# Kernel optimization log

Hardware: AMD Instinct MI355X
Metric: run time of the kernel (lower is better)

## Reference

```python
import jax, jax.numpy as jnp
import numpy as np

B, S, D, H, FF = 2, 2048, 1024, 16, 4096
DH = D // H  # head dim


def _layernorm(x, g, b, eps=1e-5):
    m = x.mean(-1, keepdims=True)
    v = ((x - m) ** 2).mean(-1, keepdims=True)
    return (x - m) / jnp.sqrt(v + eps) * g + b


def setup_inputs() -> dict:
    key = jax.random.key(0)
    ks = jax.random.split(key, 10)
    s = 0.02
    return {
        "x": jax.random.normal(ks[0], (B, S, D), jnp.float32),
        "y": jax.random.normal(ks[1], (B, S, D), jnp.float32),
        "z": jax.random.normal(ks[2], (B, S, D), jnp.float32),
        "mask": jnp.ones((B, 1, S, S), jnp.int32),
        "Wq": jax.random.normal(ks[3], (D, D), jnp.float32) * s,
        "bq": jnp.zeros((D,), jnp.float32),
        "Wk": jax.random.normal(ks[4], (D, D), jnp.float32) * s,
        "bk": jnp.zeros((D,), jnp.float32),
        "Wv": jax.random.normal(ks[5], (D, D), jnp.float32) * s,
        "bv": jnp.zeros((D,), jnp.float32),
        "Wo": jax.random.normal(ks[6], (D, D), jnp.float32) * s,
        "bo": jnp.zeros((D,), jnp.float32),
        "W1": jax.random.normal(ks[7], (D, FF), jnp.float32) * s,
        "b1": jnp.zeros((FF,), jnp.float32),
        "W2": jax.random.normal(ks[8], (FF, D), jnp.float32) * s,
        "b2": jnp.zeros((D,), jnp.float32),
        "ln_g": jnp.ones((D,), jnp.float32),
        "ln_b": jnp.zeros((D,), jnp.float32),
    }


def reference(x, y, z, mask, Wq, bq, Wk, bk, Wv, bv, Wo, bo, W1, b1, W2, b2, ln_g, ln_b):
    q = (x @ Wq + bq).reshape(B, S, H, DH)
    k = (y @ Wk + bk).reshape(B, S, H, DH)
    v = (z @ Wv + bv).reshape(B, S, H, DH)
    # scores: [B, H, Q, K]
    scores = jnp.einsum('bqhl,bkhl->bhqk', q, k) / (DH ** 0.5)
    scores = jnp.where(mask == 0, jnp.float32(-1e10), scores)
    # NOTE: source softmaxes over dim=2 (the query axis) -- faithful.
    p = jax.nn.softmax(scores, axis=2)
    # Source einsum 'bhqk,bvhl->bvhl' sums p over q,k -> per-(b,h) scalar scaling v.
    s_bh = p.sum(axis=(2, 3))  # [B, H]
    att = s_bh[:, None, :, None] * v  # [B, S, H, DH]
    att = att.reshape(B, S, D) @ Wo + bo
    # shared AddAndNorm (same LayerNorm params used twice); dropout = identity (eval)
    h1 = _layernorm(z + att, ln_g, ln_b)
    ff = jax.nn.relu(h1 @ W1 + b1) @ W2 + b2
    return _layernorm(h1 + ff, ln_g, ln_b)
```

## Files before the change

kernel.cpp:

```cpp
#include <hip/hip_runtime.h>

static constexpr int kB = 2, kS = 2048, kD = 1024, kFF = 4096;
static constexpr int kM = kB * kS;
static constexpr size_t MB = 1u << 20;

typedef __attribute__((ext_vector_type(8))) short short8;
typedef __attribute__((ext_vector_type(8))) unsigned short ushort8;
typedef __attribute__((ext_vector_type(4))) float f32x4;

__device__ __forceinline__ unsigned short f2bf(float f) {
  union { float f; unsigned int u; } c; c.f = f;
  unsigned int u = c.u;
  unsigned int r = u + 0x7FFFu + ((u >> 16) & 1u);
  return (unsigned short)(r >> 16);
}

__device__ __forceinline__ float bf2f(unsigned short b) {
  union { unsigned int u; float f; } c;
  c.u = ((unsigned int)b) << 16;
  return c.f;
}

__device__ __forceinline__ void gload_lds16(const void* g, void* l) {
  __builtin_amdgcn_global_load_lds(
      (const __attribute__((address_space(1))) void*)g,
      (__attribute__((address_space(3))) void*)l, 16, 0, 0);
}

__device__ __forceinline__ void do_ct64(
    const float* __restrict__ W, unsigned short* __restrict__ Wt,
    int K, int N, float scale, int ntN, int b, float (*tile)[65]) {
  const int nb = (b % ntN) * 64, kb = (b / ntN) * 64;
  const int tx = threadIdx.x & 15, ty = threadIdx.x >> 4;
#pragma unroll
  for (int p = 0; p < 4; ++p) {
    const int r = ty + 16 * p;
    float4 v = *(const float4*)(W + (size_t)(kb + r) * N + nb + tx * 4);
    tile[r][tx * 4 + 0] = v.x;
    tile[r][tx * 4 + 1] = v.y;
    tile[r][tx * 4 + 2] = v.z;
    tile[r][tx * 4 + 3] = v.w;
  }
  __syncthreads();
#pragma unroll
  for (int p = 0; p < 4; ++p) {
    const int n = ty + 16 * p;
    ushort4 o;
    o.x = f2bf(tile[tx * 4 + 0][n] * scale);
    o.y = f2bf(tile[tx * 4 + 1][n] * scale);
    o.z = f2bf(tile[tx * 4 + 2][n] * scale);
    o.w = f2bf(tile[tx * 4 + 3][n] * scale);
    *(ushort4*)(Wt + (size_t)(nb + n) * K + kb + tx * 4) = o;
  }
}

__global__ __launch_bounds__(256) void prep_kernel(
    const float* __restrict__ Wo, const float* __restrict__ Wv,
    const float* __restrict__ W1, const float* __restrict__ W2,
    const float* __restrict__ bv,
    unsigned short* __restrict__ WoT, unsigned short* __restrict__ WvBf,
    unsigned short* __restrict__ W1T, unsigned short* __restrict__ W2T,
    float* __restrict__ bprt) {
  __shared__ float tile[64][65];
  const int b = blockIdx.x;
  if (b < 256) {
    do_ct64(Wo, WoT, kD, kD, (float)kS, 16, b, tile);
  } else if (b < 1280) {
    do_ct64(W1, W1T, kD, kFF, 1.0f, 64, b - 256, tile);
  } else if (b < 2304) {
    do_ct64(W2, W2T, kFF, kD, 1.0f, 16, b - 1280, tile);
  } else if (b < 3328) {
    const int i = ((b - 2304) * 256 + threadIdx.x) * 4;
    float4 v = *(const float4*)(Wv + i);
    ushort4 o;
    o.x = f2bf(v.x); o.y = f2bf(v.y); o.z = f2bf(v.z); o.w = f2bf(v.w);
    *(ushort4*)(WvBf + i) = o;
  } else {
    const int bb = b - 3328, t = threadIdx.x;
    const int c = t * 4;
    float4 acc = {0.f, 0.f, 0.f, 0.f};
#pragma unroll
    for (int r = 0; r < 8; ++r) {
      const int f = bb * 8 + r;
      const float s = bv[f];
      float4 w = *(const float4*)(Wo + (size_t)f * 1024 + c);
      acc.x = fmaf(s, w.x, acc.x);
      acc.y = fmaf(s, w.y, acc.y);
      acc.z = fmaf(s, w.z, acc.z);
      acc.w = fmaf(s, w.w, acc.w);
    }
    *(float4*)(bprt + (size_t)bb * 1024 + c) = acc;
  }
}

__global__ __launch_bounds__(256) void combine_wc4_fin_kernel(
    const unsigned short* __restrict__ P, unsigned short* __restrict__ Wt,
    const float* __restrict__ bprt, const float* __restrict__ bo,
    float* __restrict__ bc) {
  const int i = (blockIdx.x * 256 + threadIdx.x) * 4;
  const int MN = 1024 * 1024;
  ushort4 s0 = *(const ushort4*)(P + i);
  ushort4 s1 = *(const ushort4*)(P + MN + i);
  ushort4 s2 = *(const ushort4*)(P + 2 * MN + i);
  ushort4 s3 = *(const ushort4*)(P + 3 * MN + i);
  const int row = i >> 10, col = i & 1023;
  float v0 = bf2f(s0.x) + bf2f(s1.x) + bf2f(s2.x) + bf2f(s3.x) + (row == col + 0 ? 1.0f : 0.0f);
  float v1 = bf2f(s0.y) + bf2f(s1.y) + bf2f(s2.y) + bf2f(s3.y) + (row == col + 1 ? 1.0f : 0.0f);
  float v2 = bf2f(s0.z) + bf2f(s1.z) + bf2f(s2.z) + bf2f(s3.z) + (row == col + 2 ? 1.0f : 0.0f);
  float v3 = bf2f(s0.w) + bf2f(s1.w) + bf2f(s2.w) + bf2f(s3.w) + (row == col + 3 ? 1.0f : 0.0f);
  ushort4 o; o.x = f2bf(v0); o.y = f2bf(v1); o.z = f2bf(v2); o.w = f2bf(v3);
  *(ushort4*)(Wt + i) = o;
  if (blockIdx.x < 4) {
    const int n = blockIdx.x * 256 + threadIdx.x;
    float acc = 0.0f;
#pragma unroll 8
    for (int bb = 0; bb < 128; ++bb) acc += bprt[(size_t)bb * 1024 + n];
    bc[n] = 2048.0f * acc + bo[n];
  }
}

template <int OUT_BF16, int RELU, int A_F32>
__global__ __launch_bounds__(256, 4) void gemm_bt(
    const void* __restrict__ A, const unsigned short* __restrict__ Bt,
    const float* __restrict__ bias, void* __restrict__ Cout,
    int M, int N, int K, int nXtiles, int nTilesPerSplit, int kSplitLen,
    size_t cStride, int cr, int cc) {
  __shared__ __align__(16) unsigned short sA[128 * 64];
  __shared__ __align__(16) unsigned short sB[128 * 64];
  const unsigned short* Ab = (const unsigned short*)A;
  const float* Af = (const float*)A;
  const int tid = threadIdx.x;
  const int wave = tid >> 6, lane = tid & 63;
  const int wr = wave >> 1, wc = wave & 1;

  const int x = blockIdx.x & 7, j = blockIdx.x >> 3;
  const int bpc = cr * cc;
  const int chunkIdx = x + 8 * (j / bpc);
  const int w = j % bpc;
  const int chunksPerSplit = nTilesPerSplit / bpc;
  const int split = chunkIdx / chunksPerSplit;
  const int cL = chunkIdx % chunksPerSplit;
  const int cpr = nXtiles / cc;
  const int m0 = ((cL / cpr) * cr + w / cc) * 128;
  const int n0 = ((cL % cpr) * cc + w % cc) * 128;
  const int kBeg = split * kSplitLen, kEnd = kBeg + kSplitLen;

  const int srow = lane >> 3;
  const int scol = ((lane & 7) ^ srow) * 8;

  f32x4 acc[4][4] = {};

  for (int k0 = kBeg; k0 < kEnd; k0 += 64) {
    if constexpr (A_F32) {
      float4 pa[4][2];
#pragma unroll
      for (int i = 0; i < 4; ++i) {
        const int chunk = i * 4 + wave;
        const int rr = chunk * 8 + srow;
        const float* az = Af + (size_t)(m0 + rr) * K + (k0 + scol);
        pa[i][0] = *(const float4*)az;
        pa[i][1] = *(const float4*)(az + 4);
      }
#pragma unroll
      for (int i = 0; i < 4; ++i) {
        const int chunk = i * 4 + wave;
        short8 cv;
        cv[0] = (short)f2bf(pa[i][0].x); cv[1] = (short)f2bf(pa[i][0].y);
        cv[2] = (short)f2bf(pa[i][0].z); cv[3] = (short)f2bf(pa[i][0].w);
        cv[4] = (short)f2bf(pa[i][1].x); cv[5] = (short)f2bf(pa[i][1].y);
        cv[6] = (short)f2bf(pa[i][1].z); cv[7] = (short)f2bf(pa[i][1].w);
        *(short8*)&sA[chunk * 512 + lane * 8] = cv;
      }
    } else {
#pragma unroll
      for (int i = 0; i < 4; ++i) {
        const int chunk = i * 4 + wave;
        const int rr = chunk * 8 + srow;
        gload_lds16(Ab + (size_t)(m0 + rr) * K + (k0 + scol), &sA[chunk * 512]);
      }
    }
#pragma unroll
    for (int i = 0; i < 4; ++i) {
      const int chunk = i * 4 + wave;
      const int rr = chunk * 8 + srow;
      gload_lds16(Bt + (size_t)(n0 + rr) * K + (k0 + scol), &sB[chunk * 512]);
    }
    __syncthreads();
#pragma unroll
    for (int kk = 0; kk < 64; kk += 32) {
      const int kcol = kk + (lane >> 4) * 8;
      const int kswz = (lane & 7) * 8;
      short8 af[4], bfr[4];
#pragma unroll
      for (int m = 0; m < 4; ++m)
        af[m] = *(const short8*)&sA[(wr * 64 + m * 16 + (lane & 15)) * 64 + (kcol ^ kswz)];
#pragma unroll
      for (int n = 0; n < 4; ++n)
        bfr[n] = *(const short8*)&sB[(wc * 64 + n * 16 + (lane & 15)) * 64 + (kcol ^ kswz)];
#pragma unroll
      for (int m = 0; m < 4; ++m)
#pragma unroll
        for (int n = 0; n < 4; ++n)
          acc[m][n] = __builtin_amdgcn_mfma_f32_16x16x32_bf16(af[m], bfr[n], acc[m][n], 0, 0, 0);
    }
    __syncthreads();
  }

  const int cl = lane & 15, rg = lane >> 4;
  const float* bptr = (split == 0) ? bias : nullptr;
#pragma unroll
  for (int n = 0; n < 4; ++n) {
    const int col = n0 + wc * 64 + n * 16 + cl;
    const float bias_v = bptr ? bptr[col] : 0.0f;
#pragma unroll
    for (int m = 0; m < 4; ++m) {
      const int rbase = m0 + wr * 64 + m * 16 + rg * 4;
#pragma unroll
      for (int j2 = 0; j2 < 4; ++j2) {
        float v = acc[m][n][j2] + bias_v;
        if (RELU) v = fmaxf(v, 0.0f);
        const size_t idx = split * cStride + (size_t)(rbase + j2) * N + col;
        if (OUT_BF16)
          ((unsigned short*)Cout)[idx] = f2bf(v);
        else
          ((float*)Cout)[idx] = v;
      }
    }
  }
}

__global__ __launch_bounds__(256) void ln4_wave_kernel(
    const unsigned short* __restrict__ P, size_t pStr,
    const float* __restrict__ gg, const float* __restrict__ bb,
    unsigned short* __restrict__ Hb) {
  const int wave = threadIdx.x >> 6, lane = threadIdx.x & 63;
  const int row = blockIdx.x * 4 + wave;
  const size_t rbase = (size_t)row * 1024;
  float a[16];
#pragma unroll
  for (int sw = 0; sw < 2; ++sw) {
    const size_t idx = rbase + sw * 512 + lane * 8;
    ushort8 v0 = *(const ushort8*)(P + idx);
    ushort8 v1 = *(const ushort8*)(P + pStr + idx);
    ushort8 v2 = *(const ushort8*)(P + 2 * pStr + idx);
    ushort8 v3 = *(const ushort8*)(P + 3 * pStr + idx);
#pragma unroll
    for (int j = 0; j < 8; ++j)
      a[sw * 8 + j] = bf2f(v0[j]) + bf2f(v1[j]) + bf2f(v2[j]) + bf2f(v3[j]);
  }
  float s = 0.f, ss = 0.f;
#pragma unroll
  for (int j = 0; j < 16; ++j) { s += a[j]; ss += a[j] * a[j]; }
#pragma unroll
  for (int off = 32; off > 0; off >>= 1) {
    s += __shfl_down(s, off);
    ss += __shfl_down(ss, off);
  }
  s = __shfl(s, 0);
  ss = __shfl(ss, 0);
  const float mean = s * (1.0f / 1024.0f);
  const float rstd = rsqrtf(ss * (1.0f / 1024.0f) - mean * mean + 1e-5f);
#pragma unroll
  for (int sw = 0; sw < 2; ++sw) {
    const int cbase = sw * 512 + lane * 8;
    float4 g0 = *(const float4*)(gg + cbase);
    float4 g1 = *(const float4*)(gg + cbase + 4);
    float4 b0 = *(const float4*)(bb + cbase);
    float4 b1 = *(const float4*)(bb + cbase + 4);
    const float* gp0 = &g0.x; const float* gp1 = &g1.x;
    const float* bp0 = &b0.x; const float* bp1 = &b1.x;
    ushort8 o;
#pragma unroll
    for (int j = 0; j < 4; ++j) {
      o[j]     = f2bf((a[sw * 8 + j]     - mean) * rstd * gp0[j] + bp0[j]);
      o[4 + j] = f2bf((a[sw * 8 + 4 + j] - mean) * rstd * gp1[j] + bp1[j]);
    }
    *(ushort8*)(Hb + rbase + cbase) = o;
  }
}

__global__ __launch_bounds__(256) void ln_fin_wave_kernel(
    const unsigned short* __restrict__ Res, const unsigned short* __restrict__ P,
    size_t pStr, const float* __restrict__ gg, const float* __restrict__ bb,
    float* __restrict__ out) {
  const int wave = threadIdx.x >> 6, lane = threadIdx.x & 63;
  const int row = blockIdx.x * 4 + wave;
  const size_t rbase = (size_t)row * 1024;
  float a[16];
#pragma unroll
  for (int sw = 0; sw < 2; ++sw) {
    const size_t idx = rbase + sw * 512 + lane * 8;
    ushort8 rv = *(const ushort8*)(Res + idx);
    ushort8 v0 = *(const ushort8*)(P + idx);
    ushort8 v1 = *(const ushort8*)(P + pStr + idx);
    ushort8 v2 = *(const ushort8*)(P + 2 * pStr + idx);
    ushort8 v3 = *(const ushort8*)(P + 3 * pStr + idx);
#pragma unroll
    for (int j = 0; j < 8; ++j)
      a[sw * 8 + j] = bf2f(rv[j]) + bf2f(v0[j]) + bf2f(v1[j]) + bf2f(v2[j]) + bf2f(v3[j]);
  }
  float s = 0.f, ss = 0.f;
#pragma unroll
  for (int j = 0; j < 16; ++j) { s += a[j]; ss += a[j] * a[j]; }
#pragma unroll
  for (int off = 32; off > 0; off >>= 1) {
    s += __shfl_down(s, off);
    ss += __shfl_down(ss, off);
  }
  s = __shfl(s, 0);
  ss = __shfl(ss, 0);
  const float mean = s * (1.0f / 1024.0f);
  const float rstd = rsqrtf(ss * (1.0f / 1024.0f) - mean * mean + 1e-5f);
#pragma unroll
  for (int sw = 0; sw < 2; ++sw) {
    const int cbase = sw * 512 + lane * 8;
    float4 g0 = *(const float4*)(gg + cbase);
    float4 g1 = *(const float4*)(gg + cbase + 4);
    float4 b0 = *(const float4*)(bb + cbase);
    float4 b1 = *(const float4*)(bb + cbase + 4);
    const float* gp0 = &g0.x; const float* gp1 = &g1.x;
    const float* bp0 = &b0.x; const float* bp1 = &b1.x;
    float4 o0, o1;
    float* op0 = &o0.x; float* op1 = &o1.x;
#pragma unroll
    for (int j = 0; j < 4; ++j) {
      op0[j] = (a[sw * 8 + j]     - mean) * rstd * gp0[j] + bp0[j];
      op1[j] = (a[sw * 8 + 4 + j] - mean) * rstd * gp1[j] + bp1[j];
    }
    *(float4*)(out + rbase + cbase) = o0;
    *(float4*)(out + rbase + cbase + 4) = o1;
  }
}

extern "C" void kernel_launch(void* const* d_in, const int* in_sizes, int n_in,
                              void* d_out, int out_size, void* d_ws, size_t ws_size,
                              hipStream_t stream) {
  const float* z  = (const float*)d_in[2];
  const float* Wv = (const float*)d_in[8];
  const float* bv = (const float*)d_in[9];
  const float* Wo = (const float*)d_in[10];
  const float* bo = (const float*)d_in[11];
  const float* W1 = (const float*)d_in[12];
  const float* b1 = (const float*)d_in[13];
  const float* W2 = (const float*)d_in[14];
  const float* b2 = (const float*)d_in[15];
  const float* lng = (const float*)d_in[16];
  const float* lnb = (const float*)d_in[17];
  float* out = (float*)d_out;

  char* ws = (char*)d_ws;
  unsigned short* a1   = (unsigned short*)(ws + 0 * MB);
  unsigned short* attP = (unsigned short*)(ws + 32 * MB);
  unsigned short* ffP  = (unsigned short*)(ws + 32 * MB);
  unsigned short* W2T  = (unsigned short*)(ws + 64 * MB);
  unsigned short* wcpB = (unsigned short*)(ws + 72 * MB);
  unsigned short* WoT  = (unsigned short*)(ws + 88 * MB);
  unsigned short* WvBf = (unsigned short*)(ws + 90 * MB);
  unsigned short* WcT  = (unsigned short*)(ws + 92 * MB);
  float*          bc   = (float*)(ws + 94 * MB);
  float*          bprt = (float*)(ws + 94 * MB + 65536);
  unsigned short* h1bf = (unsigned short*)(ws + 96 * MB);
  unsigned short* W1T  = (unsigned short*)(ws + 104 * MB);

  const size_t pStr = (size_t)kM * kD;
  const size_t wStr = (size_t)kD * kD;

  prep_kernel<<<dim3(3456), dim3(256), 0, stream>>>(
      Wo, Wv, W1, W2, bv, WoT, WvBf, W1T, W2T, bprt);

  gemm_bt<1, 0, 0><<<dim3(256), dim3(256), 0, stream>>>(
      WoT, WvBf, nullptr, wcpB, kD, kD, kD, kD / 128, 64, 256, wStr, 8, 4);

  combine_wc4_fin_kernel<<<dim3(1024), dim3(256), 0, stream>>>(
      wcpB, WcT, bprt, bo, bc);

  gemm_bt<1, 0, 1><<<dim3(1024), dim3(256), 0, stream>>>(
      z, WcT, bc, attP, kM, kD, kD, kD / 128, 256, 256, pStr, 8, 8);

  ln4_wave_kernel<<<dim3(kM / 4), dim3(256), 0, stream>>>(
      attP, pStr, lng, lnb, h1bf);

  gemm_bt<1, 1, 0><<<dim3(1024), dim3(256), 0, stream>>>(
      h1bf, W1T, b1, a1, kM, kFF, kD, kFF / 128, 1024, kD, 0, 16, 8);

  gemm_bt<1, 0, 0><<<dim3(1024), dim3(256), 0, stream>>>(
      a1, W2T, b2, ffP, kM, kD, kFF, kD / 128, 256, kFF / 4, pStr, 16, 8);

  ln_fin_wave_kernel<<<dim3(kM / 4), dim3(256), 0, stream>>>(
      h1bf, ffP, pStr, lng, lnb, out);
}
```

Before: 145.6 us.

## Add 256x128 wide-tile GEMM kernel for main activation GEMMs

Adds a gemm_wide kernel that computes 256x128 output tiles per block, with each wave holding an 8x4 grid of MFMA accumulators. The three large GEMMs (attention projection from fp32 z, FFN up with ReLU, FFN down) now use it with half as many blocks and adjusted block-swizzle parameters. The goal is more arithmetic per LDS load and less re-reading of the B operand. In exchange, accumulator registers double and launch_bounds drops to 2 blocks per SIMD, so occupancy is lower. The original gemm_bt loses its fp32-A path and is kept only for the small weight-combine GEMM.

```diff
diff --git a/kernel.cpp b/kernel.cpp
--- a/kernel.cpp
+++ b/kernel.cpp
@@ -128,7 +128,6 @@
   __shared__ __align__(16) unsigned short sA[128 * 64];
   __shared__ __align__(16) unsigned short sB[128 * 64];
   const unsigned short* Ab = (const unsigned short*)A;
-  const float* Af = (const float*)A;
   const int tid = threadIdx.x;
   const int wave = tid >> 6, lane = tid & 63;
   const int wr = wave >> 1, wc = wave & 1;
@@ -151,54 +150,142 @@
   f32x4 acc[4][4] = {};
 
   for (int k0 = kBeg; k0 < kEnd; k0 += 64) {
+#pragma unroll
+    for (int i = 0; i < 4; ++i) {
+      const int chunk = i * 4 + wave;
+      const int rr = chunk * 8 + srow;
+      gload_lds16(Ab + (size_t)(m0 + rr) * K + (k0 + scol), &sA[chunk * 512]);
+      gload_lds16(Bt + (size_t)(n0 + rr) * K + (k0 + scol), &sB[chunk * 512]);
+    }
+    __syncthreads();
+#pragma unroll
+    for (int kk = 0; kk < 64; kk += 32) {
+      const int kcol = kk + (lane >> 4) * 8;
+      const int kswz = (lane & 7) * 8;
+      short8 af[4], bfr[4];
+#pragma unroll
+      for (int m = 0; m < 4; ++m)
+        af[m] = *(const short8*)&sA[(wr * 64 + m * 16 + (lane & 15)) * 64 + (kcol ^ kswz)];
+#pragma unroll
+      for (int n = 0; n < 4; ++n)
+        bfr[n] = *(const short8*)&sB[(wc * 64 + n * 16 + (lane & 15)) * 64 + (kcol ^ kswz)];
+#pragma unroll
+      for (int m = 0; m < 4; ++m)
+#pragma unroll
+        for (int n = 0; n < 4; ++n)
+          acc[m][n] = __builtin_amdgcn_mfma_f32_16x16x32_bf16(af[m], bfr[n], acc[m][n], 0, 0, 0);
+    }
+    __syncthreads();
+  }
+
+  const int cl = lane & 15, rg = lane >> 4;
+  const float* bptr = (split == 0) ? bias : nullptr;
+#pragma unroll
+  for (int n = 0; n < 4; ++n) {
+    const int col = n0 + wc * 64 + n * 16 + cl;
+    const float bias_v = bptr ? bptr[col] : 0.0f;
+#pragma unroll
+    for (int m = 0; m < 4; ++m) {
+      const int rbase = m0 + wr * 64 + m * 16 + rg * 4;
+#pragma unroll
+      for (int j2 = 0; j2 < 4; ++j2) {
+        float v = acc[m][n][j2] + bias_v;
+        if (RELU) v = fmaxf(v, 0.0f);
+        const size_t idx = split * cStride + (size_t)(rbase + j2) * N + col;
+        if (OUT_BF16)
+          ((unsigned short*)Cout)[idx] = f2bf(v);
+        else
+          ((float*)Cout)[idx] = v;
+      }
+    }
+  }
+}
+
+template <int OUT_BF16, int RELU, int A_F32>
+__global__ __launch_bounds__(256, 2) void gemm_wide(
+    const void* __restrict__ A, const unsigned short* __restrict__ Bt,
+    const float* __restrict__ bias, void* __restrict__ Cout,
+    int M, int N, int K, int nXtiles, int nTilesPerSplit, int kSplitLen,
+    size_t cStride, int cr, int cc) {
+  __shared__ __align__(16) unsigned short sA[256 * 64];
+  __shared__ __align__(16) unsigned short sB[128 * 64];
+  const unsigned short* Ab = (const unsigned short*)A;
+  const float* Af = (const float*)A;
+  const int tid = threadIdx.x;
+  const int wave = tid >> 6, lane = tid & 63;
+  const int wr = wave >> 1, wc = wave & 1;
+  const int l15 = lane & 15, l7 = lane & 7, l4 = lane >> 4;
+
+  const int x = blockIdx.x & 7, j = blockIdx.x >> 3;
+  const int bpc = cr * cc;
+  const int chunkIdx = x + 8 * (j / bpc);
+  const int w = j % bpc;
+  const int chunksPerSplit = nTilesPerSplit / bpc;
+  const int split = chunkIdx / chunksPerSplit;
+  const int cL = chunkIdx % chunksPerSplit;
+  const int cpr = nXtiles / cc;
+  const int m0 = ((cL / cpr) * cr + w / cc) * 256;
+  const int n0 = ((cL % cpr) * cc + w % cc) * 128;
+  const int kBeg = split * kSplitLen, kEnd = kBeg + kSplitLen;
+
+  const int srow = lane >> 3;
+  const int scol = (l7 ^ srow) * 8;
+
+  f32x4 acc[8][4] = {};
+
+  for (int k0 = kBeg; k0 < kEnd; k0 += 64) {
+#pragma unroll
+    for (int i = 0; i < 4; ++i) {
+      const int chunk = i * 4 + wave;
+      const int rr = chunk * 8 + srow;
+      gload_lds16(Bt + (size_t)(n0 + rr) * K + (k0 + scol), &sB[chunk * 512]);
+    }
     if constexpr (A_F32) {
-      float4 pa[4][2];
-#pragma unroll
-      for (int i = 0; i < 4; ++i) {
-        const int chunk = i * 4 + wave;
-        const int rr = chunk * 8 + srow;
-        const float* az = Af + (size_t)(m0 + rr) * K + (k0 + scol);
-        pa[i][0] = *(const float4*)az;
-        pa[i][1] = *(const float4*)(az + 4);
-      }
-#pragma unroll
-      for (int i = 0; i < 4; ++i) {
-        const int chunk = i * 4 + wave;
-        short8 cv;
-        cv[0] = (short)f2bf(pa[i][0].x); cv[1] = (short)f2bf(pa[i][0].y);
-        cv[2] = (short)f2bf(pa[i][0].z); cv[3] = (short)f2bf(pa[i][0].w);
-        cv[4] = (short)f2bf(pa[i][1].x); cv[5] = (short)f2bf(pa[i][1].y);
-        cv[6] = (short)f2bf(pa[i][1].z); cv[7] = (short)f2bf(pa[i][1].w);
-        *(short8*)&sA[chunk * 512 + lane * 8] = cv;
+#pragma unroll
+      for (int h = 0; h < 2; ++h) {
+        float4 pa[4][2];
+#pragma unroll
+        for (int i = 0; i < 4; ++i) {
+          const int chunk = (h * 4 + i) * 4 + wave;
+          const int rr = chunk * 8 + srow;
+          const float* az = Af + (size_t)(m0 + rr) * K + (k0 + scol);
+          pa[i][0] = *(const float4*)az;
+          pa[i][1] = *(const float4*)(az + 4);
+        }
+#pragma unroll
+        for (int i = 0; i < 4; ++i) {
+          const int chunk = (h * 4 + i) * 4 + wave;
+          short8 cv;
+          cv[0] = (short)f2bf(pa[i][0].x); cv[1] = (short)f2bf(pa[i][0].y);
+          cv[2] = (short)f2bf(pa[i][0].z); cv[3] = (short)f2bf(pa[i][0].w);
+          cv[4] = (short)f2bf(pa[i][1].x); cv[5] = (short)f2bf(pa[i][1].y);
+          cv[6] = (short)f2bf(pa[i][1].z); cv[7] = (short)f2bf(pa[i][1].w);
+          *(short8*)&sA[chunk * 512 + lane * 8] = cv;
+        }
       }
     } else {
 #pragma unroll
-      for (int i = 0; i < 4; ++i) {
+      for (int i = 0; i < 8; ++i) {
         const int chunk = i * 4 + wave;
         const int rr = chunk * 8 + srow;
         gload_lds16(Ab + (size_t)(m0 + rr) * K + (k0 + scol), &sA[chunk * 512]);
       }
     }
-#pragma unroll
-    for (int i = 0; i < 4; ++i) {
-      const int chunk = i * 4 + wave;
-      const int rr = chunk * 8 + srow;
-      gload_lds16(Bt + (size_t)(n0 + rr) * K + (k0 + scol), &sB[chunk * 512]);
-    }
     __syncthreads();
 #pragma unroll
     for (int kk = 0; kk < 64; kk += 32) {
-      const int kcol = kk + (lane >> 4) * 8;
-      const int kswz = (lane & 7) * 8;
-      short8 af[4], bfr[4];
-#pragma unroll
-      for (int m = 0; m < 4; ++m)
-        af[m] = *(const short8*)&sA[(wr * 64 + m * 16 + (lane & 15)) * 64 + (kcol ^ kswz)];
+      const int kcol = kk + l4 * 8;
+      const int kswz = l7 * 8;
+      const int kr = kcol ^ kswz;
+      short8 af[8], bfr[4];
+#pragma unroll
+      for (int m = 0; m < 8; ++m)
+        af[m] = *(const short8*)&sA[(wr * 128 + m * 16 + l15) * 64 + kr];
 #pragma unroll
       for (int n = 0; n < 4; ++n)
-        bfr[n] = *(const short8*)&sB[(wc * 64 + n * 16 + (lane & 15)) * 64 + (kcol ^ kswz)];
-#pragma unroll
-      for (int m = 0; m < 4; ++m)
+        bfr[n] = *(const short8*)&sB[(wc * 64 + n * 16 + l15) * 64 + kr];
+#pragma unroll
+      for (int m = 0; m < 8; ++m)
 #pragma unroll
         for (int n = 0; n < 4; ++n)
           acc[m][n] = __builtin_amdgcn_mfma_f32_16x16x32_bf16(af[m], bfr[n], acc[m][n], 0, 0, 0);
@@ -206,15 +293,14 @@
     __syncthreads();
   }
 
-  const int cl = lane & 15, rg = lane >> 4;
   const float* bptr = (split == 0) ? bias : nullptr;
 #pragma unroll
   for (int n = 0; n < 4; ++n) {
-    const int col = n0 + wc * 64 + n * 16 + cl;
+    const int col = n0 + wc * 64 + n * 16 + l15;
     const float bias_v = bptr ? bptr[col] : 0.0f;
 #pragma unroll
-    for (int m = 0; m < 4; ++m) {
-      const int rbase = m0 + wr * 64 + m * 16 + rg * 4;
+    for (int m = 0; m < 8; ++m) {
+      const int rbase = m0 + wr * 128 + m * 16 + l4 * 4;
 #pragma unroll
       for (int j2 = 0; j2 < 4; ++j2) {
         float v = acc[m][n][j2] + bias_v;
@@ -374,17 +460,17 @@
   combine_wc4_fin_kernel<<<dim3(1024), dim3(256), 0, stream>>>(
       wcpB, WcT, bprt, bo, bc);
 
-  gemm_bt<1, 0, 1><<<dim3(1024), dim3(256), 0, stream>>>(
-      z, WcT, bc, attP, kM, kD, kD, kD / 128, 256, 256, pStr, 8, 8);
+  gemm_wide<1, 0, 1><<<dim3(512), dim3(256), 0, stream>>>(
+      z, WcT, bc, attP, kM, kD, kD, kD / 128, 128, 256, pStr, 4, 8);
 
   ln4_wave_kernel<<<dim3(kM / 4), dim3(256), 0, stream>>>(
       attP, pStr, lng, lnb, h1bf);
 
-  gemm_bt<1, 1, 0><<<dim3(1024), dim3(256), 0, stream>>>(
-      h1bf, W1T, b1, a1, kM, kFF, kD, kFF / 128, 1024, kD, 0, 16, 8);
-
-  gemm_bt<1, 0, 0><<<dim3(1024), dim3(256), 0, stream>>>(
-      a1, W2T, b2, ffP, kM, kD, kFF, kD / 128, 256, kFF / 4, pStr, 16, 8);
+  gemm_wide<1, 1, 0><<<dim3(512), dim3(256), 0, stream>>>(
+      h1bf, W1T, b1, a1, kM, kFF, kD, kFF / 128, 512, kD, 0, 4, 16);
+
+  gemm_wide<1, 0, 0><<<dim3(512), dim3(256), 0, stream>>>(
+      a1, W2T, b2, ffP, kM, kD, kFF, kD / 128, 128, kFF / 4, pStr, 4, 8);
 
   ln_fin_wave_kernel<<<dim3(kM / 4), dim3(256), 0, stream>>>(
       h1bf, ffP, pStr, lng, lnb, out);
```

New measurement: 158.1 us. +8.6%, slower.

## Use 256x256-tile 8-wave pipelined GEMM kernel for FFN up-projection

Applied to the files above, without the earlier changes.

Replaces the 128x128-tile gemm for h1@W1 (M=4096,N=4096,K=1024) with a new 512-thread kernel that computes 256x256 output tiles using double-buffered LDS staging, XOR-swizzled LDS layout, quarter-tile interleaving of loads and MFMA, and s_setprio around MFMA bursts. Larger tiles are meant to raise arithmetic intensity and reduce global/LDS traffic per FLOP, and the fine-grained staging overlaps next-tile loads with compute. The launch uses 256 blocks, one per CU at occupancy 1, so latency hiding depends entirely on the explicit schedule; the block remap with chunked grouping aims at L2 locality.

```diff
diff --git a/kernel.cpp b/kernel.cpp
--- a/kernel.cpp
+++ b/kernel.cpp
@@ -229,6 +229,137 @@
   }
 }
 
+template <int RELU>
+__global__ __launch_bounds__(512, 1) void gemm256v3(
+    const unsigned short* __restrict__ A, const unsigned short* __restrict__ Bt,
+    const float* __restrict__ bias, unsigned short* __restrict__ Cout,
+    int M, int N, int K, int nXtiles, int cr, int cc) {
+  __shared__ __align__(16) unsigned short sA[2][256 * 64];
+  __shared__ __align__(16) unsigned short sB[2][256 * 64];
+  const int tid = threadIdx.x;
+  const int wid = tid >> 6, lane = tid & 63;
+  const int wr = wid >> 2, wq = wid & 3;
+  const int l15 = lane & 15, l7 = lane & 7, l4 = lane >> 4;
+
+  const int x = blockIdx.x & 7, j = blockIdx.x >> 3;
+  const int bpc = cr * cc;
+  const int chunkIdx = x + 8 * (j / bpc);
+  const int w = j % bpc;
+  const int cpr = nXtiles / cc;
+  const int m0 = ((chunkIdx / cpr) * cr + w / cc) * 256;
+  const int n0 = ((chunkIdx % cpr) * cc + w % cc) * 256;
+
+  const int srow = lane >> 3;
+  const int sOff = ((l7 ^ srow) << 3);
+
+  auto stageA = [&](int buf, int tk, int u) {
+#pragma unroll
+    for (int q = 0; q < 2; ++q) {
+      const int base = q * 128 + u * 64 + wid * 8;
+      gload_lds16(A + (size_t)(m0 + base + srow) * K + tk * 64 + sOff,
+                  &sA[buf][base * 64]);
+    }
+  };
+  auto stageB = [&](int buf, int tk, int nh) {
+    const int rb = (wid >> 1) * 64 + nh * 32 + (wid & 1) * 16;
+#pragma unroll
+    for (int rr = 0; rr < 16; rr += 8) {
+      gload_lds16(Bt + (size_t)(n0 + rb + rr + srow) * K + tk * 64 + sOff,
+                  &sB[buf][(rb + rr) * 64]);
+    }
+  };
+
+  f32x4 acc[8][4] = {};
+  const int nt = K >> 6;
+
+  short8 a0[4][2], a1[4][2], b0[2][2], b1[2][2];
+
+#define RD_A(DST, BUF, MH)                                                    \
+  {                                                                           \
+    _Pragma("unroll") for (int fm = 0; fm < 4; ++fm) {                        \
+      const int ro = (wr * 128 + (MH) * 64 + fm * 16 + l15) * 64;             \
+      DST[fm][0] = *(const short8*)&sA[BUF][ro + ((l4 ^ l7) << 3)];           \
+      DST[fm][1] = *(const short8*)&sA[BUF][ro + ((((4 + l4)) ^ l7) << 3)];   \
+    }                                                                         \
+  }
+#define RD_B(DST, BUF, NH)                                                    \
+  {                                                                           \
+    _Pragma("unroll") for (int fn = 0; fn < 2; ++fn) {                        \
+      const int ro = (wq * 64 + (NH) * 32 + fn * 16 + l15) * 64;              \
+      DST[fn][0] = *(const short8*)&sB[BUF][ro + ((l4 ^ l7) << 3)];           \
+      DST[fn][1] = *(const short8*)&sB[BUF][ro + ((((4 + l4)) ^ l7) << 3)];   \
+    }                                                                         \
+  }
+#define MMA_Q(AF, BF, MH, NH)                                                 \
+  {                                                                           \
+    __builtin_amdgcn_s_setprio(1);                                            \
+    _Pragma("unroll") for (int fm = 0; fm < 4; ++fm)                          \
+    _Pragma("unroll") for (int fn = 0; fn < 2; ++fn) {                        \
+      acc[(MH) * 4 + fm][(NH) * 2 + fn] = __builtin_amdgcn_mfma_f32_16x16x32_bf16( \
+          AF[fm][0], BF[fn][0], acc[(MH) * 4 + fm][(NH) * 2 + fn], 0, 0, 0);  \
+      acc[(MH) * 4 + fm][(NH) * 2 + fn] = __builtin_amdgcn_mfma_f32_16x16x32_bf16( \
+          AF[fm][1], BF[fn][1], acc[(MH) * 4 + fm][(NH) * 2 + fn], 0, 0, 0);  \
+    }                                                                         \
+    __builtin_amdgcn_s_setprio(0);                                            \
+  }
+#define BAR asm volatile("s_barrier" ::: "memory")
+#define VM(N) asm volatile("s_waitcnt vmcnt(" #N ")" ::: "memory")
+
+  stageA(0, 0, 0); stageB(0, 0, 0);
+  stageB(0, 0, 1); stageA(0, 0, 1);
+  VM(4);
+  BAR;
+
+  for (int t = 0; t < nt; ++t) {
+    const int cb = t & 1, nb = cb ^ 1;
+    const bool more = (t + 1) < nt;
+    if (more) { stageA(nb, t + 1, 0); stageB(nb, t + 1, 0); }
+    RD_A(a0, cb, 0); RD_B(b0, cb, 0);
+    if (more) VM(6); else VM(2);
+    BAR;
+    MMA_Q(a0, b0, 0, 0);
+    BAR;
+    if (more) stageB(nb, t + 1, 1);
+    RD_B(b1, cb, 1);
+    if (more) VM(6); else VM(0);
+    BAR;
+    MMA_Q(a0, b1, 0, 1);
+    BAR;
+    if (more) stageA(nb, t + 1, 1);
+    RD_A(a1, cb, 1);
+    BAR;
+    MMA_Q(a1, b1, 1, 1);
+    BAR;
+    if (more) VM(4);
+    BAR;
+    MMA_Q(a1, b0, 1, 0);
+    BAR;
+  }
+#undef RD_A
+#undef RD_B
+#undef MMA_Q
+#undef BAR
+#undef VM
+
+  const int colB = n0 + wq * 64;
+  const int rowB = m0 + wr * 128 + l4 * 4;
+#pragma unroll
+  for (int fn = 0; fn < 4; ++fn) {
+    const int col = colB + fn * 16 + l15;
+    const float bias_v = bias[col];
+#pragma unroll
+    for (int fm = 0; fm < 8; ++fm) {
+      const int row = rowB + fm * 16;
+#pragma unroll
+      for (int j2 = 0; j2 < 4; ++j2) {
+        float v = acc[fm][fn][j2] + bias_v;
+        if (RELU) v = fmaxf(v, 0.0f);
+        Cout[(size_t)(row + j2) * N + col] = f2bf(v);
+      }
+    }
+  }
+}
+
 __global__ __launch_bounds__(256) void ln4_wave_kernel(
     const unsigned short* __restrict__ P, size_t pStr,
     const float* __restrict__ gg, const float* __restrict__ bb,
@@ -380,8 +511,8 @@
   ln4_wave_kernel<<<dim3(kM / 4), dim3(256), 0, stream>>>(
       attP, pStr, lng, lnb, h1bf);
 
-  gemm_bt<1, 1, 0><<<dim3(1024), dim3(256), 0, stream>>>(
-      h1bf, W1T, b1, a1, kM, kFF, kD, kFF / 128, 1024, kD, 0, 16, 8);
+  gemm256v3<1><<<dim3(256), dim3(512), 0, stream>>>(
+      h1bf, W1T, b1, a1, kM, kFF, kD, kFF / 256, 4, 8);
 
   gemm_bt<1, 0, 0><<<dim3(1024), dim3(256), 0, stream>>>(
       a1, W2T, b2, ffP, kM, kD, kFF, kD / 128, 256, kFF / 4, pStr, 16, 8);
```

Result: slower. 165.2 us (+13.5%).
